# Performance work log

Measured on AMD Instinct MI355X. Metric: run time of the kernel, lower is better.

Reference implementation:

```python
import jax, jax.numpy as jnp
import numpy as np


def setup_inputs() -> dict:
    key = jax.random.key(0)
    kq, kc = jax.random.split(key)
    query = jax.random.normal(kq, (64, 768), dtype=jnp.float32)
    corpus = jax.random.normal(kc, (500000, 768), dtype=jnp.float32)
    return {"query": query, "corpus": corpus, "k": 16}


def reference(query, corpus, k):
    # cosine similarity: (q @ c.T) / (|q|[:,None] * |c|[None,:])  -> [B, N]
    sim = jnp.einsum("bd,nd->bn", query, corpus)
    qn = jnp.linalg.norm(query, axis=1)   # [B]
    cn = jnp.linalg.norm(corpus, axis=1)  # [N]
    sim = sim / (qn[:, None] * cn[None, :])
    # top-k most similar corpus entries per query (largest=True)
    values, indices = jax.lax.top_k(sim, k)  # [B, k], [B, k]
    return values, indices
```

## Files before the change

### kernel.cpp

```cpp
#include <hip/hip_runtime.h>
#include <hip/hip_bf16.h>

#define D 768
#define NQ 64
#define RT 16
#define SIMGRID 256
#define SIMTPB 256
#define KSTEPS 24
#define NMW 4096
#define NS 8
#define CANDCAP 256
#define MARGIN 4e-3f

#define QLDS 98304
#define CTILE 24576
#define LDS_BYTES (QLDS + 2 * CTILE + 2 * RT * 4)

typedef float    f32x4 __attribute__((ext_vector_type(4)));
typedef _Float16 h16x8 __attribute__((ext_vector_type(8)));

typedef const void __attribute__((address_space(1)))* gas_ptr;
typedef void __attribute__((address_space(3)))* las_ptr;

__device__ __forceinline__ unsigned short f2bf(float f) {
    unsigned int u = __float_as_uint(f);
    return (unsigned short)((u + 0x7fffu + ((u >> 16) & 1u)) >> 16);
}
__device__ __forceinline__ float bf2f(unsigned short b) {
    return __uint_as_float(((unsigned int)b) << 16);
}

__device__ __forceinline__ bool kbetter(float v1, int i1, float v2, int i2) {
    return (v1 > v2) || (v1 == v2 && i1 < i2);
}

__device__ __forceinline__ void topk_insert(float (&tv)[16], int (&ti)[16], float v, int idx) {
    if (!kbetter(v, idx, tv[15], ti[15])) return;
    tv[15] = v; ti[15] = idx;
    #pragma unroll
    for (int s = 15; s >= 1; --s) {
        bool sw = kbetter(tv[s], ti[s], tv[s-1], ti[s-1]);
        float av = sw ? tv[s] : tv[s-1];
        float bv = sw ? tv[s-1] : tv[s];
        int   ai = sw ? ti[s] : ti[s-1];
        int   bi = sw ? ti[s-1] : ti[s];
        tv[s-1] = av; tv[s] = bv; ti[s-1] = ai; ti[s] = bi;
    }
}

__device__ __forceinline__ void bitonic16(float (&v)[16], int (&ix)[16]) {
    #pragma unroll
    for (int d = 8; d >= 1; d >>= 1) {
        #pragma unroll
        for (int i = 0; i < 16; ++i) {
            if ((i & d) == 0) {
                int j = i | d;
                bool sw = kbetter(v[j], ix[j], v[i], ix[i]);
                float av = sw ? v[j] : v[i];
                float bv = sw ? v[i] : v[j];
                int   ai = sw ? ix[j] : ix[i];
                int   bi = sw ? ix[i] : ix[j];
                v[i] = av; v[j] = bv; ix[i] = ai; ix[j] = bi;
            }
        }
    }
}

__device__ __forceinline__ void lane_merge(float (&v)[16], int (&ix)[16], int mask) {
    float pv[16]; int pix[16];
    #pragma unroll
    for (int i = 0; i < 16; ++i) {
        pv[i]  = __shfl_xor(v[15 - i], mask);
        pix[i] = __shfl_xor(ix[15 - i], mask);
    }
    #pragma unroll
    for (int i = 0; i < 16; ++i) {
        if (kbetter(pv[i], pix[i], v[i], ix[i])) { v[i] = pv[i]; ix[i] = pix[i]; }
    }
    bitonic16(v, ix);
}

__device__ __forceinline__ void sort64(float& v, int& ix, int l) {
    #pragma unroll
    for (int k = 2; k <= 64; k <<= 1) {
        #pragma unroll
        for (int j = k >> 1; j >= 1; j >>= 1) {
            float ov = __shfl_xor(v, j);
            int   oi = __shfl_xor(ix, j);
            bool dirDesc = ((l & k) == 0);
            bool lower   = ((l & j) == 0);
            bool takeBetter = (lower == dirDesc);
            bool ob = kbetter(ov, oi, v, ix);
            if (takeBetter == ob) { v = ov; ix = oi; }
        }
    }
}

__device__ __forceinline__ bool kbetterD(double v1, int i1, double v2, int i2) {
    return (v1 > v2) || (v1 == v2 && i1 < i2);
}

__device__ __forceinline__ void topk_insertD(double (&tv)[16], int (&ti)[16], double v, int idx) {
    if (!kbetterD(v, idx, tv[15], ti[15])) return;
    tv[15] = v; ti[15] = idx;
    #pragma unroll
    for (int s = 15; s >= 1; --s) {
        bool sw = kbetterD(tv[s], ti[s], tv[s-1], ti[s-1]);
        double av = sw ? tv[s] : tv[s-1];
        double bv = sw ? tv[s-1] : tv[s];
        int    ai = sw ? ti[s] : ti[s-1];
        int    bi = sw ? ti[s-1] : ti[s];
        tv[s-1] = av; tv[s] = bv; ti[s-1] = ai; ti[s] = bi;
    }
}

__device__ __forceinline__ void bitonic16D(double (&v)[16], int (&ix)[16]) {
    #pragma unroll
    for (int d = 8; d >= 1; d >>= 1) {
        #pragma unroll
        for (int i = 0; i < 16; ++i) {
            if ((i & d) == 0) {
                int j = i | d;
                bool sw = kbetterD(v[j], ix[j], v[i], ix[i]);
                double av = sw ? v[j] : v[i];
                double bv = sw ? v[i] : v[j];
                int    ai = sw ? ix[j] : ix[i];
                int    bi = sw ? ix[i] : ix[j];
                v[i] = av; v[j] = bv; ix[i] = ai; ix[j] = bi;
            }
        }
    }
}

__device__ __forceinline__ void lane_mergeD(double (&v)[16], int (&ix)[16], int mask) {
    double pv[16]; int pix[16];
    #pragma unroll
    for (int i = 0; i < 16; ++i) {
        pv[i]  = __shfl_xor(v[15 - i], mask);
        pix[i] = __shfl_xor(ix[15 - i], mask);
    }
    #pragma unroll
    for (int i = 0; i < 16; ++i) {
        if (kbetterD(pv[i], pix[i], v[i], ix[i])) { v[i] = pv[i]; ix[i] = pix[i]; }
    }
    bitonic16D(v, ix);
}

__global__ __launch_bounds__(256)
void prep_kernel(const float* __restrict__ query, _Float16* __restrict__ qpk,
                 float* __restrict__ qn) {
    int b = blockIdx.x, t = threadIdx.x;
    const float* row = query + b * D;
    float vals[3]; float s = 0.f;
    #pragma unroll
    for (int j = 0; j < 3; ++j) { vals[j] = row[t + 256 * j]; s += vals[j] * vals[j]; }
    #pragma unroll
    for (int m = 1; m < 64; m <<= 1) s += __shfl_xor(s, m);
    __shared__ float ws4[4];
    if ((t & 63) == 0) ws4[t >> 6] = s;
    __syncthreads();
    float qnorm = sqrtf(ws4[0] + ws4[1] + ws4[2] + ws4[3]);
    int qf = b >> 4;
    #pragma unroll
    for (int j = 0; j < 3; ++j) {
        int col = t + 256 * j;
        float vn = vals[j] / qnorm;
        qn[b * D + col] = vn;
        int ks = col >> 5, unit = (col >> 3) & 3, sub = col & 7;
        int lane = (b & 15) + unit * 16;
        qpk[(((size_t)ks * 4 + qf) * 64 + lane) * 8 + sub] = (_Float16)vn;
    }
}

__global__ __launch_bounds__(SIMTPB, 1)
void sim_kernel(const float* __restrict__ corpus,
                const _Float16* __restrict__ qpk,
                unsigned short* __restrict__ simout, int N, int NTILES) {
    extern __shared__ __align__(16) char smem[];
    const _Float16* qlds = (const _Float16*)smem;
    char*  ct = smem + QLDS;
    float* cn = (float*)(smem + QLDS + 2 * CTILE);

    int t = threadIdx.x, w = t >> 6, l = t & 63;
    int row = t >> 4, seg = t & 15;
    int qf = w;

    #pragma unroll
    for (int j = 0; j < 24; ++j) {
        int idx = t + 256 * j;
        __builtin_amdgcn_global_load_lds((gas_ptr)(const void*)(qpk + (size_t)idx * 8),
                                         (las_ptr)(void*)(smem + (size_t)idx * 16), 16, 0, 0);
    }
    __syncthreads();

    int b = blockIdx.x;
    int q0 = NTILES / SIMGRID, r0 = NTILES % SIMGRID;
    int t0 = b * q0 + min(b, r0);
    int cnt = q0 + (b < r0 ? 1 : 0);

    float4 stg[12];

    auto LOADT = [&](int tile) {
        long grow = (long)tile * RT + row; if (grow > N - 1) grow = N - 1;
        const float* p = corpus + (size_t)grow * D + seg * 48;
        #pragma unroll
        for (int j = 0; j < 12; ++j) stg[j] = *(const float4*)(p + j * 4);
    };

    auto CVTW = [&](int buf) {
        char* base = ct + buf * CTILE;
        float ps = 0.f;
        #pragma unroll
        for (int j = 0; j < 6; ++j) {
            float4 a = stg[2 * j], c = stg[2 * j + 1];
            ps += a.x * a.x + a.y * a.y + a.z * a.z + a.w * a.w;
            ps += c.x * c.x + c.y * c.y + c.z * c.z + c.w * c.w;
            h16x8 hv;
            hv[0] = (_Float16)a.x; hv[1] = (_Float16)a.y; hv[2] = (_Float16)a.z; hv[3] = (_Float16)a.w;
            hv[4] = (_Float16)c.x; hv[5] = (_Float16)c.y; hv[6] = (_Float16)c.z; hv[7] = (_Float16)c.w;
            int off = (row * 1536 + seg * 96 + j * 16) ^ ((row & 7) << 4);
            *(h16x8*)(base + off) = hv;
        }
        ps += __shfl_xor(ps, 1); ps += __shfl_xor(ps, 2);
        ps += __shfl_xor(ps, 4); ps += __shfl_xor(ps, 8);
        if (seg == 0) cn[buf * RT + row] = ps;
    };

    auto COMPUTE = [&](int tile, int buf) {
        const char* base = ct + buf * CTILE;
        f32x4 acc = (f32x4)(0.f);
        #pragma unroll
        for (int ks = 0; ks < KSTEPS; ++ks) {
            h16x8 qh = *(const h16x8*)(qlds + (((size_t)ks * 4 + qf) * 64 + l) * 8);
            int cb = ((l & 15) * 1536 + ks * 64 + (l >> 4) * 16) ^ ((l & 7) << 4);
            h16x8 ch = *(const h16x8*)(base + cb);
            acc = __builtin_amdgcn_mfma_f32_16x16x32_f16(qh, ch, acc, 0, 0, 0);
        }
        int nl = l & 15;
        long n = (long)tile * RT + nl;
        float inv = 1.0f / sqrtf(cn[buf * RT + nl]);
        if (n < N) {
            ushort4 pk;
            pk.x = f2bf(acc[0] * inv); pk.y = f2bf(acc[1] * inv);
            pk.z = f2bf(acc[2] * inv); pk.w = f2bf(acc[3] * inv);
            *(ushort4*)(simout + n * NQ + qf * 16 + (l >> 4) * 4) = pk;
        }
    };

    LOADT(t0);
    CVTW(0);
    __syncthreads();

    for (int i = 0; i < cnt; ++i) {
        if (i + 1 < cnt) LOADT(t0 + i + 1);
        COMPUTE(t0 + i, i & 1);
        if (i + 1 < cnt) CVTW((i + 1) & 1);
        __syncthreads();
    }
}

__global__ __launch_bounds__(256)
void mergeA_kernel(const unsigned short* __restrict__ simout, float2* __restrict__ candA, int N) {
    int t = threadIdx.x, w = t >> 6, l = t & 63;
    int ww = blockIdx.x * 4 + w;
    int chunk = (N + NMW - 1) / NMW;
    int n0 = ww * chunk, n1 = min(N, n0 + chunk);

    float tv[16]; int ti[16];
    #pragma unroll
    for (int s = 0; s < 16; ++s) { tv[s] = -INFINITY; ti[s] = 0x7fffffff; }

    int n = n0;
    for (; n + 8 <= n1; n += 8) {
        float v[8];
        #pragma unroll
        for (int j = 0; j < 8; ++j) v[j] = bf2f(simout[(size_t)(n + j) * NQ + l]);
        #pragma unroll
        for (int j = 0; j < 8; ++j) topk_insert(tv, ti, v[j], n + j);
    }
    for (; n < n1; ++n) topk_insert(tv, ti, bf2f(simout[(size_t)n * NQ + l]), n);

    float2* dst = candA + ((size_t)l * NMW + ww) * 16;
    #pragma unroll
    for (int s = 0; s < 16; ++s) dst[s] = make_float2(tv[s], __int_as_float(ti[s]));
}

__global__ __launch_bounds__(256)
void merge1_kernel(const float2* __restrict__ cand, float2* __restrict__ cand2, int NWV) {
    int q = blockIdx.x >> 3, seg = blockIdx.x & (NS - 1);
    int t = threadIdx.x, w = t >> 6, l = t & 63;
    int total = NWV * 16;
    int chunk = (total + NS - 1) / NS;
    int e0 = seg * chunk, e1 = min(total, e0 + chunk);
    const float2* src = cand + (size_t)q * total;
    float tv[16]; int ti[16];
    #pragma unroll
    for (int s = 0; s < 16; ++s) { tv[s] = -INFINITY; ti[s] = 0x7fffffff; }
    for (int e = e0 + t; e < e1; e += 256) {
        float2 ce = src[e];
        topk_insert(tv, ti, ce.x, __float_as_int(ce.y));
    }
    lane_merge(tv, ti, 1);  lane_merge(tv, ti, 2);  lane_merge(tv, ti, 4);
    lane_merge(tv, ti, 8);  lane_merge(tv, ti, 16); lane_merge(tv, ti, 32);
    __shared__ float2 stage[64];
    if (l == 0) {
        #pragma unroll
        for (int s = 0; s < 16; ++s) stage[w * 16 + s] = make_float2(tv[s], __int_as_float(ti[s]));
    }
    __syncthreads();
    if (t < 64) {
        float2 ce = stage[t];
        float v = ce.x; int ix = __float_as_int(ce.y);
        sort64(v, ix, t);
        if (t < 16) cand2[((size_t)q * NS + seg) * 16 + t] = make_float2(v, __int_as_float(ix));
    }
}

__global__ __launch_bounds__(64)
void merge2t_kernel(const float2* __restrict__ cand2, float* __restrict__ thr,
                    int* __restrict__ cnt) {
    int q = blockIdx.x, l = threadIdx.x;
    const float2* src = cand2 + (size_t)q * (NS * 16);
    float2 a = src[l], b = src[l + 64];
    float v1 = a.x; int i1 = __float_as_int(a.y);
    float v2 = b.x; int i2 = __float_as_int(b.y);
    sort64(v1, i1, l);
    sort64(v2, i2, l);
    float sv = __shfl(v2, (l - 16) & 63);
    int   si = __shfl(i2, (l - 16) & 63);
    float mv = (l < 16) ? v1 : ((l < 32) ? sv : -INFINITY);
    int   mi = (l < 16) ? i1 : ((l < 32) ? si : 0x7fffffff);
    sort64(mv, mi, l);
    if (l == 15) {
        thr[q] = mv - MARGIN;
        cnt[q] = 0;
    }
}

__global__ __launch_bounds__(256)
void filter_kernel(const unsigned short* __restrict__ simout, const float* __restrict__ thr,
                   int* __restrict__ cnt, int* __restrict__ candx, int N) {
    int t = threadIdx.x, w = t >> 6, l = t & 63;
    int wid = blockIdx.x * 4 + w;
    int nwaves = gridDim.x * 4;
    float th = thr[l];
    for (int n = wid; n < N; n += nwaves) {
        float v = bf2f(simout[(size_t)n * NQ + l]);
        if (v >= th) {
            int s = atomicAdd(&cnt[l], 1);
            if (s < CANDCAP) candx[l * CANDCAP + s] = n;
        }
    }
}

__global__ __launch_bounds__(256)
void exact_kernel(const float* __restrict__ corpus, const float* __restrict__ qn,
                  const int* __restrict__ cnt, const int* __restrict__ candx,
                  float* __restrict__ out, int N) {
    int q = blockIdx.x, t = threadIdx.x, w = t >> 6, l = t & 63;
    int m = min(cnt[q], CANDCAP);
    __shared__ double vals[CANDCAP];
    __shared__ int    idxs[CANDCAP];

    const float* qr = qn + q * D;
    for (int c = w; c < m; c += 4) {
        int n = candx[q * CANDCAP + c];
        const float* cr = corpus + (size_t)n * D;
        double acc = 0.0, cs = 0.0;
        #pragma unroll
        for (int j = 0; j < D / 64; ++j) {
            double cv = (double)cr[l + j * 64];
            acc += (double)qr[l + j * 64] * cv;
            cs  += cv * cv;
        }
        #pragma unroll
        for (int msk = 1; msk < 64; msk <<= 1) {
            acc += __shfl_xor(acc, msk);
            cs  += __shfl_xor(cs, msk);
        }
        if (l == 0) { vals[c] = acc / sqrt(cs); idxs[c] = n; }
    }
    __syncthreads();

    if (w == 0) {
        double tv[16]; int ti[16];
        #pragma unroll
        for (int s = 0; s < 16; ++s) { tv[s] = -1e300; ti[s] = 0x7fffffff; }
        for (int r = 0; r < CANDCAP / 64; ++r) {
            int e = l + r * 64;
            if (e < m) topk_insertD(tv, ti, vals[e], idxs[e]);
        }
        lane_mergeD(tv, ti, 1);  lane_mergeD(tv, ti, 2);  lane_mergeD(tv, ti, 4);
        lane_mergeD(tv, ti, 8);  lane_mergeD(tv, ti, 16); lane_mergeD(tv, ti, 32);
        if (l == 0) {
            #pragma unroll
            for (int s = 0; s < 16; ++s) {
                out[q * 16 + s]           = (float)tv[s];
                out[NQ * 16 + q * 16 + s] = (float)ti[s];
            }
        }
    }
}

extern "C" void kernel_launch(void* const* d_in, const int* in_sizes, int n_in,
                              void* d_out, int out_size, void* d_ws, size_t ws_size,
                              hipStream_t stream) {
    const float* query  = (const float*)d_in[0];
    const float* corpus = (const float*)d_in[1];
    int N      = in_sizes[1] / D;
    int NTILES = (N + RT - 1) / RT;

    char* ws = (char*)d_ws;
    _Float16* qpk = (_Float16*)ws;
    float* qn     = (float*)(ws + 98304);
    unsigned short* simout = (unsigned short*)(ws + 98304 + 196608);
    size_t simBytes = (size_t)NTILES * RT * NQ * sizeof(unsigned short);
    char* p = ws + 98304 + 196608 + simBytes;
    float2* candA = (float2*)p;
    size_t candABytes = (size_t)NQ * NMW * 16 * sizeof(float2);
    float2* cand2 = (float2*)(p + candABytes);
    float*  thr   = (float*)(p + candABytes + 65536);
    int*    cnt   = (int*)(p + candABytes + 65536 + 256);
    int*    candx = (int*)(p + candABytes + 65536 + 512);
    float* out = (float*)d_out;

    (void)hipFuncSetAttribute((const void*)sim_kernel,
                              hipFuncAttributeMaxDynamicSharedMemorySize, LDS_BYTES);

    prep_kernel<<<NQ, 256, 0, stream>>>(query, qpk, qn);
    sim_kernel<<<SIMGRID, SIMTPB, LDS_BYTES, stream>>>(corpus, qpk, simout, N, NTILES);
    mergeA_kernel<<<NMW / 4, 256, 0, stream>>>(simout, candA, N);
    merge1_kernel<<<NQ * NS, 256, 0, stream>>>(candA, cand2, NMW);
    merge2t_kernel<<<NQ, 64, 0, stream>>>(cand2, thr, cnt);
    filter_kernel<<<1024, 256, 0, stream>>>(simout, thr, cnt, candx, N);
    exact_kernel<<<NQ, 256, 0, stream>>>(corpus, qn, cnt, candx, out, N);
}
```

Measured before the change: 625.9 us.

## Widen sim kernel to 16 waves with split-K and two-deep register prefetch

The similarity kernel now runs 1024 threads per block instead of 256. The 16 waves split the K dimension four ways, and partial accumulators are reduced through an LDS scratch area. Corpus tile loads are issued two tiles ahead into alternating register sets, so more global-load latency is hidden and more loads are in flight per CU. The cost is extra LDS traffic and two barriers per tile for the split-K reduction, plus higher register and LDS pressure.

```diff
diff --git a/kernel.cpp b/kernel.cpp
--- a/kernel.cpp
+++ b/kernel.cpp
@@ -5,19 +5,22 @@
 #define NQ 64
 #define RT 16
 #define SIMGRID 256
-#define SIMTPB 256
-#define KSTEPS 24
+#define SIMTPB 1024
 #define NMW 4096
 #define NS 8
 #define CANDCAP 256
 #define MARGIN 4e-3f
 
-#define QLDS 98304
-#define CTILE 24576
-#define LDS_BYTES (QLDS + 2 * CTILE + 2 * RT * 4)
+#define LDS_Q      0
+#define LDS_TILE   98304
+#define TILE_B     24576
+#define LDS_SCR    147456
+#define LDS_CN     159744
+#define LDS_BYTES  159872
 
 typedef float    f32x4 __attribute__((ext_vector_type(4)));
 typedef _Float16 h16x8 __attribute__((ext_vector_type(8)));
+typedef _Float16 h16x4 __attribute__((ext_vector_type(4)));
 
 typedef const void __attribute__((address_space(1)))* gas_ptr;
 typedef void __attribute__((address_space(3)))* las_ptr;
@@ -172,90 +175,106 @@
     }
 }
 
-__global__ __launch_bounds__(SIMTPB, 1)
+__global__ __launch_bounds__(SIMTPB, 4)
 void sim_kernel(const float* __restrict__ corpus,
                 const _Float16* __restrict__ qpk,
                 unsigned short* __restrict__ simout, int N, int NTILES) {
     extern __shared__ __align__(16) char smem[];
     const _Float16* qlds = (const _Float16*)smem;
-    char*  ct = smem + QLDS;
-    float* cn = (float*)(smem + QLDS + 2 * CTILE);
+    char*  tiles   = smem + LDS_TILE;
+    float* scratch = (float*)(smem + LDS_SCR);
+    float* cn      = (float*)(smem + LDS_CN);
 
     int t = threadIdx.x, w = t >> 6, l = t & 63;
-    int row = t >> 4, seg = t & 15;
-    int qf = w;
-
-    #pragma unroll
-    for (int j = 0; j < 24; ++j) {
-        int idx = t + 256 * j;
+    int qf = w & 3, kq = w >> 2;
+    int row = w;
+    int n16 = l & 15, kg = l >> 4;
+
+    #pragma unroll
+    for (int j = 0; j < 6; ++j) {
+        int idx = t + SIMTPB * j;
         __builtin_amdgcn_global_load_lds((gas_ptr)(const void*)(qpk + (size_t)idx * 8),
                                          (las_ptr)(void*)(smem + (size_t)idx * 16), 16, 0, 0);
     }
-    __syncthreads();
 
     int b = blockIdx.x;
     int q0 = NTILES / SIMGRID, r0 = NTILES % SIMGRID;
     int t0 = b * q0 + min(b, r0);
     int cnt = q0 + (b < r0 ? 1 : 0);
 
-    float4 stg[12];
-
-    auto LOADT = [&](int tile) {
-        long grow = (long)tile * RT + row; if (grow > N - 1) grow = N - 1;
-        const float* p = corpus + (size_t)grow * D + seg * 48;
-        #pragma unroll
-        for (int j = 0; j < 12; ++j) stg[j] = *(const float4*)(p + j * 4);
+    auto LOADT = [&](int i, float4 (&R)[3]) {
+        long g = (long)(t0 + i) * RT + row;
+        if (g > N - 1) g = N - 1;
+        const float* p = corpus + (size_t)g * D + l * 12;
+        R[0] = *(const float4*)p;
+        R[1] = *(const float4*)(p + 4);
+        R[2] = *(const float4*)(p + 8);
     };
 
-    auto CVTW = [&](int buf) {
-        char* base = ct + buf * CTILE;
+    auto CVT = [&](float4 (&R)[3], int buf) {
+        char* base = tiles + buf * TILE_B;
         float ps = 0.f;
-        #pragma unroll
-        for (int j = 0; j < 6; ++j) {
-            float4 a = stg[2 * j], c = stg[2 * j + 1];
-            ps += a.x * a.x + a.y * a.y + a.z * a.z + a.w * a.w;
-            ps += c.x * c.x + c.y * c.y + c.z * c.z + c.w * c.w;
-            h16x8 hv;
-            hv[0] = (_Float16)a.x; hv[1] = (_Float16)a.y; hv[2] = (_Float16)a.z; hv[3] = (_Float16)a.w;
-            hv[4] = (_Float16)c.x; hv[5] = (_Float16)c.y; hv[6] = (_Float16)c.z; hv[7] = (_Float16)c.w;
-            int off = (row * 1536 + seg * 96 + j * 16) ^ ((row & 7) << 4);
-            *(h16x8*)(base + off) = hv;
-        }
-        ps += __shfl_xor(ps, 1); ps += __shfl_xor(ps, 2);
-        ps += __shfl_xor(ps, 4); ps += __shfl_xor(ps, 8);
-        if (seg == 0) cn[buf * RT + row] = ps;
+        int swz = (row & 7) << 4;
+        #pragma unroll
+        for (int j = 0; j < 3; ++j) {
+            float4 x = R[j];
+            ps += x.x * x.x + x.y * x.y + x.z * x.z + x.w * x.w;
+            h16x4 h;
+            h.x = (_Float16)x.x; h.y = (_Float16)x.y;
+            h.z = (_Float16)x.z; h.w = (_Float16)x.w;
+            int off = row * 1536 + l * 24 + j * 8;
+            *(h16x4*)(base + (off ^ swz)) = h;
+        }
+        #pragma unroll
+        for (int m = 1; m < 64; m <<= 1) ps += __shfl_xor(ps, m);
+        if (l == 0) cn[buf * RT + row] = ps;
     };
 
-    auto COMPUTE = [&](int tile, int buf) {
-        const char* base = ct + buf * CTILE;
+    auto BODY = [&](int i, float4 (&Rcons)[3], float4 (&Riss)[3]) {
+        float cnv = cn[(i & 1) * RT + n16];
+        if (i + 2 < cnt) LOADT(i + 2, Riss);
+        const char* base = tiles + (i & 1) * TILE_B;
         f32x4 acc = (f32x4)(0.f);
-        #pragma unroll
-        for (int ks = 0; ks < KSTEPS; ++ks) {
+        int cswz = (n16 & 7) << 4;
+        #pragma unroll
+        for (int s = 0; s < 6; ++s) {
+            int ks = kq * 6 + s;
             h16x8 qh = *(const h16x8*)(qlds + (((size_t)ks * 4 + qf) * 64 + l) * 8);
-            int cb = ((l & 15) * 1536 + ks * 64 + (l >> 4) * 16) ^ ((l & 7) << 4);
-            h16x8 ch = *(const h16x8*)(base + cb);
+            int cb = n16 * 1536 + ks * 64 + kg * 16;
+            h16x8 ch = *(const h16x8*)(base + (cb ^ cswz));
             acc = __builtin_amdgcn_mfma_f32_16x16x32_f16(qh, ch, acc, 0, 0, 0);
         }
-        int nl = l & 15;
-        long n = (long)tile * RT + nl;
-        float inv = 1.0f / sqrtf(cn[buf * RT + nl]);
-        if (n < N) {
-            ushort4 pk;
-            pk.x = f2bf(acc[0] * inv); pk.y = f2bf(acc[1] * inv);
-            pk.z = f2bf(acc[2] * inv); pk.w = f2bf(acc[3] * inv);
-            *(ushort4*)(simout + n * NQ + qf * 16 + (l >> 4) * 4) = pk;
+        if (i + 1 < cnt) CVT(Rcons, (i + 1) & 1);
+        asm volatile("s_waitcnt lgkmcnt(0)" ::: "memory");
+        __builtin_amdgcn_s_barrier();
+        if (kq) *(f32x4*)(scratch + ((kq - 1) * 4 + qf) * 256 + l * 4) = acc;
+        asm volatile("s_waitcnt lgkmcnt(0)" ::: "memory");
+        __builtin_amdgcn_s_barrier();
+        if (kq == 0) {
+            #pragma unroll
+            for (int p = 0; p < 3; ++p)
+                acc += *(const f32x4*)(scratch + (p * 4 + qf) * 256 + l * 4);
+            float inv = 1.0f / sqrtf(cnv);
+            long n = (long)(t0 + i) * RT + n16;
+            if (n < N) {
+                ushort4 pk;
+                pk.x = f2bf(acc[0] * inv); pk.y = f2bf(acc[1] * inv);
+                pk.z = f2bf(acc[2] * inv); pk.w = f2bf(acc[3] * inv);
+                *(ushort4*)(simout + n * NQ + qf * 16 + kg * 4) = pk;
+            }
         }
     };
 
-    LOADT(t0);
-    CVTW(0);
+    float4 RA[3], RB[3];
+    LOADT(0, RA);
+    if (cnt > 1) LOADT(1, RB);
+    CVT(RA, 0);
     __syncthreads();
 
-    for (int i = 0; i < cnt; ++i) {
-        if (i + 1 < cnt) LOADT(t0 + i + 1);
-        COMPUTE(t0 + i, i & 1);
-        if (i + 1 < cnt) CVTW((i + 1) & 1);
-        __syncthreads();
+    int i = 0;
+    while (i < cnt) {
+        BODY(i, RB, RA); ++i;
+        if (i < cnt) { BODY(i, RA, RB); ++i; }
     }
 }
 
```

Measured after the change: 606.7 us. 3.1% less time.
